# Kernel optimization log

Measured on AMD Instinct MI355X. Metric: run time of the kernel, lower is better.

Reference implementation:

```python
import jax, jax.numpy as jnp
import numpy as np

B, S, D, H = 2, 2048, 1024, 16
DK = D // H  # 64


def setup_inputs() -> dict:
    key = jax.random.key(0)
    ks = jax.random.split(key, 11)
    scale = 1.0 / np.sqrt(D)
    inp = {
        "x": jax.random.normal(ks[0], (B, S, D), dtype=jnp.float32),
        "z": jax.random.normal(ks[1], (B, S, D), dtype=jnp.float32),
        # causal mask, broadcast over batch and heads; masked_fill where mask==0
        "mask": jnp.tril(jnp.ones((1, 1, S, S), dtype=jnp.int32)),
        "wq_w": jax.random.normal(ks[2], (D, D), dtype=jnp.float32) * scale,
        "wq_b": jax.random.normal(ks[3], (D,), dtype=jnp.float32) * 0.01,
        "wk_w": jax.random.normal(ks[4], (D, D), dtype=jnp.float32) * scale,
        "wk_b": jax.random.normal(ks[5], (D,), dtype=jnp.float32) * 0.01,
        "wv_w": jax.random.normal(ks[6], (D, D), dtype=jnp.float32) * scale,
        "wv_b": jax.random.normal(ks[7], (D,), dtype=jnp.float32) * 0.01,
        "wo_w": jax.random.normal(ks[8], (D, D), dtype=jnp.float32) * scale,
        "wo_b": jax.random.normal(ks[9], (D,), dtype=jnp.float32) * 0.01,
    }
    return inp


def reference(x, z, mask, wq_w, wq_b, wk_w, wk_b, wv_w, wv_b, wo_w, wo_b):
    # torch Linear: y = x @ W.T + b
    q = x @ wq_w.T + wq_b
    k = z @ wk_w.T + wk_b
    # NOTE: faithful to source bug: value uses wk, not wv (wv is a dead param)
    v = z @ wk_w.T + wk_b

    def split_heads(t):  # [B,S,D] -> [B,H,S,DK]
        return t.reshape(B, S, H, DK).transpose(0, 2, 1, 3)

    q, k, v = split_heads(q), split_heads(k), split_heads(v)

    scores = jnp.einsum("bhqd,bhkd->bhqk", q, k) * (DK ** -0.5)
    scores = jnp.where(mask == 0, -jnp.inf, scores)
    attn_weights = jax.nn.softmax(scores, axis=-1)  # [B,H,S,S]
    atn = jnp.einsum("bhqk,bhkd->bhqd", attn_weights, v)

    concat = atn.transpose(0, 2, 1, 3).reshape(B, S, D)
    output = concat @ wo_w.T + wo_b  # dropout rate 0.0 -> identity
    concat_attn_weight = attn_weights.sum(axis=1)  # [B,S,S]
    return output, concat_attn_weight
```

## Files before the change

### kernel.cpp

```cpp
#include <hip/hip_runtime.h>

typedef __bf16 bf16_t;
typedef __bf16 bf16x4 __attribute__((ext_vector_type(4)));
typedef __bf16 bf16x8 __attribute__((ext_vector_type(8)));
typedef float  f32x4  __attribute__((ext_vector_type(4)));

#define MFMA(a, b, c) __builtin_amdgcn_mfma_f32_16x16x32_bf16((a), (b), (c), 0, 0, 0)

static constexpr int Bsz = 2, S = 2048, D = 1024, H = 16, DK = 64;
static constexpr float QSCALE = 0.125f * 1.4426950408889634f;

__device__ __forceinline__ float fexp2(float x) {
    return __builtin_amdgcn_exp2f(x);
}

__global__ __launch_bounds__(256) void cvt5(
    const float* __restrict__ x, const float* __restrict__ z,
    const float* __restrict__ wq, const float* __restrict__ wk,
    const float* __restrict__ wo,
    bf16_t* __restrict__ xb, bf16_t* __restrict__ zb,
    bf16_t* __restrict__ wqb, bf16_t* __restrict__ wkb, bf16_t* __restrict__ wob)
{
    constexpr int NXZ = Bsz * S * D / 4;
    constexpr int NW  = D * D / 4;
    int i = blockIdx.x * 256 + threadIdx.x;
    const float* s; bf16_t* d; int off;
    if (i < NXZ)                 { s = x;  d = xb;  off = i; }
    else if (i < 2 * NXZ)        { s = z;  d = zb;  off = i - NXZ; }
    else if (i < 2 * NXZ + NW)   { s = wq; d = wqb; off = i - 2 * NXZ; }
    else if (i < 2 * NXZ + 2*NW) { s = wk; d = wkb; off = i - 2 * NXZ - NW; }
    else                         { s = wo; d = wob; off = i - 2 * NXZ - 2 * NW; }
    float4 v = *(const float4*)&s[(size_t)off * 4];
    bf16x4 o;
    o[0] = (bf16_t)v.x; o[1] = (bf16_t)v.y; o[2] = (bf16_t)v.z; o[3] = (bf16_t)v.w;
    *(bf16x4*)&d[(size_t)off * 4] = o;
}

__global__ __launch_bounds__(512) void gemm_qk(
    const bf16_t* __restrict__ xA, const bf16_t* __restrict__ wqB,
    const float* __restrict__ wqb, bf16_t* __restrict__ Qc,
    const bf16_t* __restrict__ zA, const bf16_t* __restrict__ wkB,
    const float* __restrict__ wkb, bf16_t* __restrict__ Kc,
    bf16_t* __restrict__ KTout)
{
    constexpr int N = D, K = D;
    const int zi = blockIdx.z;
    const bf16_t* A    = zi ? zA  : xA;
    const bf16_t* B    = zi ? wkB : wqB;
    const float*  bias = zi ? wkb : wqb;
    bf16_t*       C    = zi ? Kc  : Qc;
    const float   sc   = zi ? 1.f : QSCALE;

    __shared__ bf16_t As[2][128][40];
    __shared__ bf16_t Bs[2][128][40];

    const int t    = threadIdx.x;
    const int wave = t >> 6, lane = t & 63;
    const int quad = lane >> 4, l15 = lane & 15;
    const int wm = (wave >> 1) * 32, wn = (wave & 1) * 64;
    const int rowbase = blockIdx.y * 128, colbase = blockIdx.x * 128;
    const int r  = t >> 2;
    const int cc = (t & 3) << 3;

    f32x4 acc[2][4];
#pragma unroll
    for (int i = 0; i < 2; ++i)
#pragma unroll
        for (int j = 0; j < 4; ++j) acc[i][j] = {0.f, 0.f, 0.f, 0.f};

    bf16x8 areg = *(const bf16x8*)&A[(size_t)(rowbase + r) * K + cc];
    bf16x8 breg = *(const bf16x8*)&B[(size_t)(colbase + r) * K + cc];
    *(bf16x8*)&As[0][r][cc] = areg;
    *(bf16x8*)&Bs[0][r][cc] = breg;
    __syncthreads();

    for (int kt = 0; kt < K; kt += 32) {
        const int cur = (kt >> 5) & 1, nxt = cur ^ 1;
        const bool more = (kt + 32) < K;
        if (more) {
            areg = *(const bf16x8*)&A[(size_t)(rowbase + r) * K + kt + 32 + cc];
            breg = *(const bf16x8*)&B[(size_t)(colbase + r) * K + kt + 32 + cc];
        }

        bf16x8 af[2], bfr[4];
#pragma unroll
        for (int mt = 0; mt < 2; ++mt)
            af[mt] = *(const bf16x8*)&As[cur][wm + mt * 16 + l15][quad * 8];
#pragma unroll
        for (int nt = 0; nt < 4; ++nt)
            bfr[nt] = *(const bf16x8*)&Bs[cur][wn + nt * 16 + l15][quad * 8];
#pragma unroll
        for (int mt = 0; mt < 2; ++mt)
#pragma unroll
            for (int nt = 0; nt < 4; ++nt)
                acc[mt][nt] = MFMA(af[mt], bfr[nt], acc[mt][nt]);

        if (more) {
            *(bf16x8*)&As[nxt][r][cc] = areg;
            *(bf16x8*)&Bs[nxt][r][cc] = breg;
        }
        __syncthreads();
    }

#pragma unroll
    for (int nt = 0; nt < 4; ++nt) {
        int col  = colbase + wn + nt * 16 + l15;
        float bv = bias[col];
#pragma unroll
        for (int mt = 0; mt < 2; ++mt) {
            int row0 = rowbase + wm + mt * 16 + quad * 4;
#pragma unroll
            for (int rr = 0; rr < 4; ++rr) {
                float v = (acc[mt][nt][rr] + bv) * sc;
                C[(size_t)(row0 + rr) * N + col] = (bf16_t)v;
                if (zi) {
                    int row = row0 + rr;
                    int bb = row >> 11, srow = row & (S - 1);
                    int hh = col >> 6,  dd   = col & 63;
                    KTout[(((size_t)bb * H + hh) * DK + dd) * S + srow] = (bf16_t)v;
                }
            }
        }
    }
}

__global__ __launch_bounds__(256) void gemm_obt(
    const bf16_t* __restrict__ A, const bf16_t* __restrict__ B,
    const float* __restrict__ bias, float* __restrict__ C)
{
    constexpr int N = D, K = D;
    __shared__ bf16_t As[2][64][40];
    __shared__ bf16_t Bs[2][128][40];

    const int t    = threadIdx.x;
    const int wave = t >> 6, lane = t & 63;
    const int quad = lane >> 4, l15 = lane & 15;
    const int wm = (wave >> 1) * 32, wn = (wave & 1) * 64;
    const int rowbase = blockIdx.y * 64, colbase = blockIdx.x * 128;
    const int r  = t >> 2;
    const int cc = (t & 3) << 3;

    f32x4 acc[2][4];
#pragma unroll
    for (int i = 0; i < 2; ++i)
#pragma unroll
        for (int j = 0; j < 4; ++j) acc[i][j] = {0.f, 0.f, 0.f, 0.f};

    bf16x8 areg  = *(const bf16x8*)&A[(size_t)(rowbase + r) * K + cc];
    bf16x8 breg0 = *(const bf16x8*)&B[(size_t)(colbase + r) * K + cc];
    bf16x8 breg1 = *(const bf16x8*)&B[(size_t)(colbase + 64 + r) * K + cc];
    *(bf16x8*)&As[0][r][cc]      = areg;
    *(bf16x8*)&Bs[0][r][cc]      = breg0;
    *(bf16x8*)&Bs[0][64 + r][cc] = breg1;
    __syncthreads();

    for (int kt = 0; kt < K; kt += 32) {
        const int cur = (kt >> 5) & 1, nxt = cur ^ 1;
        const bool more = (kt + 32) < K;
        if (more) {
            areg  = *(const bf16x8*)&A[(size_t)(rowbase + r) * K + kt + 32 + cc];
            breg0 = *(const bf16x8*)&B[(size_t)(colbase + r) * K + kt + 32 + cc];
            breg1 = *(const bf16x8*)&B[(size_t)(colbase + 64 + r) * K + kt + 32 + cc];
        }

        bf16x8 af[2], bfr[4];
#pragma unroll
        for (int mt = 0; mt < 2; ++mt)
            af[mt] = *(const bf16x8*)&As[cur][wm + mt * 16 + l15][quad * 8];
#pragma unroll
        for (int nt = 0; nt < 4; ++nt)
            bfr[nt] = *(const bf16x8*)&Bs[cur][wn + nt * 16 + l15][quad * 8];
#pragma unroll
        for (int mt = 0; mt < 2; ++mt)
#pragma unroll
            for (int nt = 0; nt < 4; ++nt)
                acc[mt][nt] = MFMA(af[mt], bfr[nt], acc[mt][nt]);

        if (more) {
            *(bf16x8*)&As[nxt][r][cc]      = areg;
            *(bf16x8*)&Bs[nxt][r][cc]      = breg0;
            *(bf16x8*)&Bs[nxt][64 + r][cc] = breg1;
        }
        __syncthreads();
    }

#pragma unroll
    for (int nt = 0; nt < 4; ++nt) {
        int col  = colbase + wn + nt * 16 + l15;
        float bv = bias[col];
#pragma unroll
        for (int mt = 0; mt < 2; ++mt) {
            int row0 = rowbase + wm + mt * 16 + quad * 4;
#pragma unroll
            for (int rr = 0; rr < 4; ++rr)
                C[(size_t)(row0 + rr) * N + col] = acc[mt][nt][rr] + bv;
        }
    }
}

__global__ __launch_bounds__(256) void attn_flash(
    const bf16_t* __restrict__ Q, const bf16_t* __restrict__ Km,
    const bf16_t* __restrict__ KT,
    bf16_t* __restrict__ Oc, float* __restrict__ il_ws)
{
    const int h = blockIdx.y, b = blockIdx.z;
    const int t = threadIdx.x;
    const int wave = t >> 6, lane = t & 63;
    const int quad = lane >> 4, l15 = lane & 15;

    __shared__ bf16_t Ks[2][64][72];
    __shared__ bf16_t KTs[2][64][72];
    __shared__ bf16_t PQ[64][72];

    const int hcol = h * DK;
    const bf16_t* KTh = KT + ((size_t)(b * H + h)) * DK * S;
    const size_t bS = (size_t)b * S;

    const int jr = (t >> 3);
    const int ce = (t & 7) * 8;
    const int iloc = wave * 16 + l15;

    for (int half = 0; half < 2; ++half) {
        const int qt = half == 0 ? (int)blockIdx.x : 31 - (int)blockIdx.x;
        const size_t qrow0 = bS + (size_t)qt * 64;

        __syncthreads();
        bf16x8 qld[2], kreg[2], ktreg[2];
#pragma unroll
        for (int p = 0; p < 2; ++p) {
            qld[p]   = *(const bf16x8*)&Q[(qrow0 + p * 32 + jr) * D + hcol + ce];
            kreg[p]  = *(const bf16x8*)&Km[(bS + p * 32 + jr) * D + hcol + ce];
            ktreg[p] = *(const bf16x8*)&KTh[(size_t)(p * 32 + jr) * S + ce];
        }
#pragma unroll
        for (int p = 0; p < 2; ++p) {
            *(bf16x8*)&PQ[p * 32 + jr][ce]     = qld[p];
            *(bf16x8*)&Ks[0][p * 32 + jr][ce]  = kreg[p];
            *(bf16x8*)&KTs[0][p * 32 + jr][ce] = ktreg[p];
        }
        __syncthreads();
        const bf16x8 qf0 = *(const bf16x8*)&PQ[wave * 16 + l15][quad * 8];
        const bf16x8 qf1 = *(const bf16x8*)&PQ[wave * 16 + l15][32 + quad * 8];

        f32x4 accO[4];
#pragma unroll
        for (int u = 0; u < 4; ++u) accO[u] = {0.f, 0.f, 0.f, 0.f};
        float l_part = 0.f;

        auto exp_pv = [&](f32x4 sv[4], int cur) {
#pragma unroll
            for (int nt = 0; nt < 4; ++nt)
#pragma unroll
                for (int r = 0; r < 4; ++r) {
                    float p = fexp2(sv[nt][r]);
                    sv[nt][r] = p;
                    l_part += p;
                }

#pragma unroll
            for (int nt = 0; nt < 4; ++nt) {
                bf16x4 pk;
                pk[0] = (bf16_t)sv[nt][0]; pk[1] = (bf16_t)sv[nt][1];
                pk[2] = (bf16_t)sv[nt][2]; pk[3] = (bf16_t)sv[nt][3];
                *(bf16x4*)&PQ[wave * 16 + l15][nt * 16 + quad * 4] = pk;
            }
            asm volatile("s_waitcnt lgkmcnt(0)" ::: "memory");

            bf16x8 pa0 = *(const bf16x8*)&PQ[wave * 16 + l15][quad * 8];
            bf16x8 pa1 = *(const bf16x8*)&PQ[wave * 16 + l15][32 + quad * 8];
#pragma unroll
            for (int u = 0; u < 4; ++u) {
                bf16x8 v0 = *(const bf16x8*)&KTs[cur][u * 16 + l15][quad * 8];
                bf16x8 v1 = *(const bf16x8*)&KTs[cur][u * 16 + l15][32 + quad * 8];
                accO[u] = MFMA(pa0, v0, accO[u]);
                accO[u] = MFMA(pa1, v1, accO[u]);
            }
        };

        for (int jt = 0; jt < qt; ++jt) {
            const int cur = jt & 1, nxt = cur ^ 1;
#pragma unroll
            for (int p = 0; p < 2; ++p) {
                kreg[p]  = *(const bf16x8*)&Km[(bS + (size_t)(jt + 1) * 64 + p * 32 + jr) * D + hcol + ce];
                ktreg[p] = *(const bf16x8*)&KTh[(size_t)(p * 32 + jr) * S + (size_t)(jt + 1) * 64 + ce];
            }

            f32x4 sv[4];
#pragma unroll
            for (int nt = 0; nt < 4; ++nt) {
                bf16x8 a0 = *(const bf16x8*)&Ks[cur][nt * 16 + l15][quad * 8];
                bf16x8 a1 = *(const bf16x8*)&Ks[cur][nt * 16 + l15][32 + quad * 8];
                f32x4 a = {0.f, 0.f, 0.f, 0.f};
                a = MFMA(a0, qf0, a);
                a = MFMA(a1, qf1, a);
                sv[nt] = a;
            }
            exp_pv(sv, cur);

#pragma unroll
            for (int p = 0; p < 2; ++p) {
                *(bf16x8*)&Ks[nxt][p * 32 + jr][ce]  = kreg[p];
                *(bf16x8*)&KTs[nxt][p * 32 + jr][ce] = ktreg[p];
            }
            __syncthreads();
        }

        {
            const int cur = qt & 1;
            f32x4 sv[4];
#pragma unroll
            for (int nt = 0; nt < 4; ++nt) {
                bf16x8 a0 = *(const bf16x8*)&Ks[cur][nt * 16 + l15][quad * 8];
                bf16x8 a1 = *(const bf16x8*)&Ks[cur][nt * 16 + l15][32 + quad * 8];
                f32x4 a = {0.f, 0.f, 0.f, 0.f};
                a = MFMA(a0, qf0, a);
                a = MFMA(a1, qf1, a);
#pragma unroll
                for (int r = 0; r < 4; ++r)
                    if ((nt * 16 + quad * 4 + r) > iloc) a[r] = -1e30f;
                sv[nt] = a;
            }
            exp_pv(sv, cur);
        }

        l_part += __shfl_xor(l_part, 16);
        l_part += __shfl_xor(l_part, 32);
        float invl = 1.f / l_part;
        float invl4[4];
#pragma unroll
        for (int r = 0; r < 4; ++r)
            invl4[r] = __shfl(invl, (quad << 4) + quad * 4 + r, 64);
#pragma unroll
        for (int u = 0; u < 4; ++u)
#pragma unroll
            for (int r = 0; r < 4; ++r)
                Oc[(qrow0 + wave * 16 + quad * 4 + r) * D + hcol + u * 16 + l15] =
                    (bf16_t)(accO[u][r] * invl4[r]);

        if (quad == 0) {
            size_t sb = ((size_t)(b * H + h)) * S + (size_t)qt * 64 + wave * 16 + l15;
            il_ws[sb] = invl;
        }
    }
}

__global__ __launch_bounds__(256) void attn_wsum(
    const bf16_t* __restrict__ Q, const bf16_t* __restrict__ Km,
    const float* __restrict__ il_ws, float* __restrict__ out2)
{
    const int jt = blockIdx.x, qt = blockIdx.y, b = blockIdx.z;
    const int t  = threadIdx.x;
    float* tile = out2 + (size_t)b * S * S + (size_t)qt * 64 * S + (size_t)jt * 64;

    if (jt > qt) {
        int r0 = t >> 2, c0 = (t & 3) * 16;
#pragma unroll
        for (int e = 0; e < 16; ++e) tile[(size_t)r0 * S + c0 + e] = 0.f;
        return;
    }

    const int wave = t >> 6, lane = t & 63;
    const int quad = lane >> 4, l15 = lane & 15;
    __shared__ bf16_t Ks[2][64][72];
    __shared__ bf16_t Qs[2][64][72];

    const int jr = (t >> 3), ce = (t & 7) * 8;
    const size_t krow = (size_t)b * S + (size_t)jt * 64;
    const size_t qrow = (size_t)b * S + (size_t)qt * 64;
    const bool diag = (jt == qt);

    f32x4 accs[4];
#pragma unroll
    for (int nt = 0; nt < 4; ++nt) accs[nt] = {0.f, 0.f, 0.f, 0.f};

    bf16x8 kreg[2], qreg[2];
#pragma unroll
    for (int p = 0; p < 2; ++p) {
        kreg[p] = *(const bf16x8*)&Km[(krow + p * 32 + jr) * D + ce];
        qreg[p] = *(const bf16x8*)&Q[(qrow + p * 32 + jr) * D + ce];
    }
#pragma unroll
    for (int p = 0; p < 2; ++p) {
        *(bf16x8*)&Ks[0][p * 32 + jr][ce] = kreg[p];
        *(bf16x8*)&Qs[0][p * 32 + jr][ce] = qreg[p];
    }
    __syncthreads();

    for (int h = 0; h < H; ++h) {
        const int cur = h & 1, nxt = cur ^ 1;

        if (h < H - 1) {
            const int hc = (h + 1) * DK;
#pragma unroll
            for (int p = 0; p < 2; ++p) {
                kreg[p] = *(const bf16x8*)&Km[(krow + p * 32 + jr) * D + hc + ce];
                qreg[p] = *(const bf16x8*)&Q[(qrow + p * 32 + jr) * D + hc + ce];
            }
        }

        bf16x8 qf0 = *(const bf16x8*)&Qs[cur][wave * 16 + l15][quad * 8];
        bf16x8 qf1 = *(const bf16x8*)&Qs[cur][wave * 16 + l15][32 + quad * 8];

        size_t mlb = ((size_t)(b * H + h)) * S + (size_t)qt * 64 + wave * 16 + quad * 4;
        f32x4 il = *(const f32x4*)&il_ws[mlb];

#pragma unroll
        for (int nt = 0; nt < 4; ++nt) {
            bf16x8 k0 = *(const bf16x8*)&Ks[cur][nt * 16 + l15][quad * 8];
            bf16x8 k1 = *(const bf16x8*)&Ks[cur][nt * 16 + l15][32 + quad * 8];
            f32x4 a = {0.f, 0.f, 0.f, 0.f};
            a = MFMA(qf0, k0, a);
            a = MFMA(qf1, k1, a);
            if (diag) {
#pragma unroll
                for (int r = 0; r < 4; ++r) {
                    int i = wave * 16 + quad * 4 + r;
                    int j = nt * 16 + l15;
                    float p = (j <= i) ? fexp2(a[r]) * il[r] : 0.f;
                    accs[nt][r] += p;
                }
            } else {
#pragma unroll
                for (int r = 0; r < 4; ++r)
                    accs[nt][r] += fexp2(a[r]) * il[r];
            }
        }

        if (h < H - 1) {
#pragma unroll
            for (int p = 0; p < 2; ++p) {
                *(bf16x8*)&Ks[nxt][p * 32 + jr][ce] = kreg[p];
                *(bf16x8*)&Qs[nxt][p * 32 + jr][ce] = qreg[p];
            }
        }
        __syncthreads();
    }

#pragma unroll
    for (int nt = 0; nt < 4; ++nt)
#pragma unroll
        for (int r = 0; r < 4; ++r)
            tile[(size_t)(wave * 16 + quad * 4 + r) * S + nt * 16 + l15] = accs[nt][r];
}

extern "C" void kernel_launch(void* const* d_in, const int* in_sizes, int n_in,
                              void* d_out, int out_size, void* d_ws, size_t ws_size,
                              hipStream_t stream)
{
    const float* x    = (const float*)d_in[0];
    const float* z    = (const float*)d_in[1];
    const float* wq_w = (const float*)d_in[3];
    const float* wq_b = (const float*)d_in[4];
    const float* wk_w = (const float*)d_in[5];
    const float* wk_b = (const float*)d_in[6];
    const float* wo_w = (const float*)d_in[9];
    const float* wo_b = (const float*)d_in[10];

    float* out  = (float*)d_out;
    float* out2 = out + (size_t)Bsz * S * D;

    float*  il_ws = (float*)d_ws;
    bf16_t* Qws   = (bf16_t*)(il_ws + (size_t)Bsz * H * S);
    bf16_t* Kws   = Qws + (size_t)Bsz * S * D;
    bf16_t* wq_bf = Kws + (size_t)Bsz * S * D;
    bf16_t* wk_bf = wq_bf + (size_t)D * D;
    bf16_t* wo_bf = wk_bf + (size_t)D * D;
    bf16_t* xb    = (bf16_t*)out;
    bf16_t* zb    = xb + (size_t)Bsz * S * D;
    bf16_t* Cc    = (bf16_t*)out2;
    bf16_t* KTws  = Cc + (size_t)Bsz * S * D;

    constexpr int CVT_BLOCKS = (2 * (Bsz * S * D / 4) + 3 * (D * D / 4)) / 256;
    cvt5<<<dim3(CVT_BLOCKS), dim3(256), 0, stream>>>(
        x, z, wq_w, wk_w, wo_w, xb, zb, wq_bf, wk_bf, wo_bf);
    gemm_qk<<<dim3(D / 128, (Bsz * S) / 128, 2), dim3(512), 0, stream>>>(
        xb, wq_bf, wq_b, Qws, zb, wk_bf, wk_b, Kws, KTws);
    attn_flash<<<dim3(S / 128, H, Bsz), dim3(256), 0, stream>>>(
        Qws, Kws, KTws, Cc, il_ws);
    gemm_obt<<<dim3(D / 128, (Bsz * S) / 64, 1), dim3(256), 0, stream>>>(
        Cc, wo_bf, wo_b, out);
    attn_wsum<<<dim3(S / 64, S / 64, Bsz), dim3(256), 0, stream>>>(
        Qws, Kws, il_ws, out2);
}
```

Measured before the change: 266.0 us.

## Fuse output projection and attention-weight sum into one launch

Merges the output-projection GEMM and the head-summed attention-weight kernel into a single launch whose block index selects which body to run. When the workspace is large enough, the concat buffer and K-transpose move into the workspace so they no longer alias out2, which makes running both tails concurrently safe. Separately, the weight-sum kernel now reads Q fragments straight from global memory into registers instead of staging them through shared memory. The aim is to cut one launch and its tail idle time and let the two tails overlap. In exchange the fused kernel reserves the larger shared-memory footprint for every block, which may lower occupancy for the weight-sum blocks.

```diff
diff --git a/kernel.cpp b/kernel.cpp
--- a/kernel.cpp
+++ b/kernel.cpp
@@ -124,19 +124,20 @@
     }
 }
 
-__global__ __launch_bounds__(256) void gemm_obt(
+__device__ __forceinline__ void obt_body(
+    int id, char* smem,
     const bf16_t* __restrict__ A, const bf16_t* __restrict__ B,
     const float* __restrict__ bias, float* __restrict__ C)
 {
     constexpr int N = D, K = D;
-    __shared__ bf16_t As[2][64][40];
-    __shared__ bf16_t Bs[2][128][40];
+    auto As = (bf16_t(*)[64][40])smem;
+    auto Bs = (bf16_t(*)[128][40])(smem + 10240);
 
     const int t    = threadIdx.x;
     const int wave = t >> 6, lane = t & 63;
     const int quad = lane >> 4, l15 = lane & 15;
     const int wm = (wave >> 1) * 32, wn = (wave & 1) * 64;
-    const int rowbase = blockIdx.y * 64, colbase = blockIdx.x * 128;
+    const int rowbase = (id >> 3) * 64, colbase = (id & 7) * 128;
     const int r  = t >> 2;
     const int cc = (t & 3) << 3;
 
@@ -198,6 +199,126 @@
     }
 }
 
+__device__ __forceinline__ void wsum_body(
+    int id, char* smem,
+    const bf16_t* __restrict__ Q, const bf16_t* __restrict__ Km,
+    const float* __restrict__ il_ws, float* __restrict__ out2)
+{
+    const int jt = id & 31, qt = (id >> 5) & 31, b = id >> 10;
+    const int t  = threadIdx.x;
+    float* tile = out2 + (size_t)b * S * S + (size_t)qt * 64 * S + (size_t)jt * 64;
+
+    if (jt > qt) {
+        int r0 = t >> 2, c0 = (t & 3) * 16;
+#pragma unroll
+        for (int e = 0; e < 16; ++e) tile[(size_t)r0 * S + c0 + e] = 0.f;
+        return;
+    }
+
+    const int wave = t >> 6, lane = t & 63;
+    const int quad = lane >> 4, l15 = lane & 15;
+    auto Ks = (bf16_t(*)[64][72])smem;
+
+    const int jr = (t >> 3), ce = (t & 7) * 8;
+    const size_t krow  = (size_t)b * S + (size_t)jt * 64;
+    const size_t qbase = ((size_t)b * S + (size_t)qt * 64 + wave * 16 + l15) * D + quad * 8;
+    const bool diag = (jt == qt);
+
+    f32x4 accs[4];
+#pragma unroll
+    for (int nt = 0; nt < 4; ++nt) accs[nt] = {0.f, 0.f, 0.f, 0.f};
+
+    bf16x8 kreg[2];
+#pragma unroll
+    for (int p = 0; p < 2; ++p)
+        kreg[p] = *(const bf16x8*)&Km[(krow + p * 32 + jr) * D + ce];
+    bf16x8 qf0 = *(const bf16x8*)&Q[qbase];
+    bf16x8 qf1 = *(const bf16x8*)&Q[qbase + 32];
+#pragma unroll
+    for (int p = 0; p < 2; ++p)
+        *(bf16x8*)&Ks[0][p * 32 + jr][ce] = kreg[p];
+    __syncthreads();
+
+    for (int h = 0; h < H; ++h) {
+        const int cur = h & 1, nxt = cur ^ 1;
+        bf16x8 qn0, qn1;
+        if (h < H - 1) {
+            const int hc = (h + 1) * DK;
+#pragma unroll
+            for (int p = 0; p < 2; ++p)
+                kreg[p] = *(const bf16x8*)&Km[(krow + p * 32 + jr) * D + hc + ce];
+            qn0 = *(const bf16x8*)&Q[qbase + hc];
+            qn1 = *(const bf16x8*)&Q[qbase + hc + 32];
+        }
+
+        size_t mlb = ((size_t)(b * H + h)) * S + (size_t)qt * 64 + wave * 16 + quad * 4;
+        f32x4 il = *(const f32x4*)&il_ws[mlb];
+
+#pragma unroll
+        for (int nt = 0; nt < 4; ++nt) {
+            bf16x8 k0 = *(const bf16x8*)&Ks[cur][nt * 16 + l15][quad * 8];
+            bf16x8 k1 = *(const bf16x8*)&Ks[cur][nt * 16 + l15][32 + quad * 8];
+            f32x4 a = {0.f, 0.f, 0.f, 0.f};
+            a = MFMA(qf0, k0, a);
+            a = MFMA(qf1, k1, a);
+            if (diag) {
+#pragma unroll
+                for (int r = 0; r < 4; ++r) {
+                    int i = wave * 16 + quad * 4 + r;
+                    int j = nt * 16 + l15;
+                    float p = (j <= i) ? fexp2(a[r]) * il[r] : 0.f;
+                    accs[nt][r] += p;
+                }
+            } else {
+#pragma unroll
+                for (int r = 0; r < 4; ++r)
+                    accs[nt][r] += fexp2(a[r]) * il[r];
+            }
+        }
+
+        if (h < H - 1) {
+#pragma unroll
+            for (int p = 0; p < 2; ++p)
+                *(bf16x8*)&Ks[nxt][p * 32 + jr][ce] = kreg[p];
+            qf0 = qn0; qf1 = qn1;
+        }
+        __syncthreads();
+    }
+
+#pragma unroll
+    for (int nt = 0; nt < 4; ++nt)
+#pragma unroll
+        for (int r = 0; r < 4; ++r)
+            tile[(size_t)(wave * 16 + quad * 4 + r) * S + nt * 16 + l15] = accs[nt][r];
+}
+
+__global__ __launch_bounds__(256) void tail_fused(
+    const bf16_t* __restrict__ Cc, const bf16_t* __restrict__ wo,
+    const float* __restrict__ wob, float* __restrict__ out,
+    const bf16_t* __restrict__ Q, const bf16_t* __restrict__ Km,
+    const float* __restrict__ il_ws, float* __restrict__ out2)
+{
+    __shared__ __align__(16) char smem[30720];
+    const int id = blockIdx.x;
+    if (id < 2048) wsum_body(id, smem, Q, Km, il_ws, out2);
+    else           obt_body(id - 2048, smem, Cc, wo, wob, out);
+}
+
+__global__ __launch_bounds__(256) void gemm_obt(
+    const bf16_t* __restrict__ A, const bf16_t* __restrict__ B,
+    const float* __restrict__ bias, float* __restrict__ C)
+{
+    __shared__ __align__(16) char smem[30720];
+    obt_body(blockIdx.x, smem, A, B, bias, C);
+}
+__global__ __launch_bounds__(256) void attn_wsum(
+    const bf16_t* __restrict__ Q, const bf16_t* __restrict__ Km,
+    const float* __restrict__ il_ws, float* __restrict__ out2)
+{
+    __shared__ __align__(16) char smem[18432];
+    wsum_body(blockIdx.x, smem, Q, Km, il_ws, out2);
+}
+
 __global__ __launch_bounds__(256) void attn_flash(
     const bf16_t* __restrict__ Q, const bf16_t* __restrict__ Km,
     const bf16_t* __restrict__ KT,
@@ -342,105 +463,6 @@
             il_ws[sb] = invl;
         }
     }
-}
-
-__global__ __launch_bounds__(256) void attn_wsum(
-    const bf16_t* __restrict__ Q, const bf16_t* __restrict__ Km,
-    const float* __restrict__ il_ws, float* __restrict__ out2)
-{
-    const int jt = blockIdx.x, qt = blockIdx.y, b = blockIdx.z;
-    const int t  = threadIdx.x;
-    float* tile = out2 + (size_t)b * S * S + (size_t)qt * 64 * S + (size_t)jt * 64;
-
-    if (jt > qt) {
-        int r0 = t >> 2, c0 = (t & 3) * 16;
-#pragma unroll
-        for (int e = 0; e < 16; ++e) tile[(size_t)r0 * S + c0 + e] = 0.f;
-        return;
-    }
-
-    const int wave = t >> 6, lane = t & 63;
-    const int quad = lane >> 4, l15 = lane & 15;
-    __shared__ bf16_t Ks[2][64][72];
-    __shared__ bf16_t Qs[2][64][72];
-
-    const int jr = (t >> 3), ce = (t & 7) * 8;
-    const size_t krow = (size_t)b * S + (size_t)jt * 64;
-    const size_t qrow = (size_t)b * S + (size_t)qt * 64;
-    const bool diag = (jt == qt);
-
-    f32x4 accs[4];
-#pragma unroll
-    for (int nt = 0; nt < 4; ++nt) accs[nt] = {0.f, 0.f, 0.f, 0.f};
-
-    bf16x8 kreg[2], qreg[2];
-#pragma unroll
-    for (int p = 0; p < 2; ++p) {
-        kreg[p] = *(const bf16x8*)&Km[(krow + p * 32 + jr) * D + ce];
-        qreg[p] = *(const bf16x8*)&Q[(qrow + p * 32 + jr) * D + ce];
-    }
-#pragma unroll
-    for (int p = 0; p < 2; ++p) {
-        *(bf16x8*)&Ks[0][p * 32 + jr][ce] = kreg[p];
-        *(bf16x8*)&Qs[0][p * 32 + jr][ce] = qreg[p];
-    }
-    __syncthreads();
-
-    for (int h = 0; h < H; ++h) {
-        const int cur = h & 1, nxt = cur ^ 1;
-
-        if (h < H - 1) {
-            const int hc = (h + 1) * DK;
-#pragma unroll
-            for (int p = 0; p < 2; ++p) {
-                kreg[p] = *(const bf16x8*)&Km[(krow + p * 32 + jr) * D + hc + ce];
-                qreg[p] = *(const bf16x8*)&Q[(qrow + p * 32 + jr) * D + hc + ce];
-            }
-        }
-
-        bf16x8 qf0 = *(const bf16x8*)&Qs[cur][wave * 16 + l15][quad * 8];
-        bf16x8 qf1 = *(const bf16x8*)&Qs[cur][wave * 16 + l15][32 + quad * 8];
-
-        size_t mlb = ((size_t)(b * H + h)) * S + (size_t)qt * 64 + wave * 16 + quad * 4;
-        f32x4 il = *(const f32x4*)&il_ws[mlb];
-
-#pragma unroll
-        for (int nt = 0; nt < 4; ++nt) {
-            bf16x8 k0 = *(const bf16x8*)&Ks[cur][nt * 16 + l15][quad * 8];
-            bf16x8 k1 = *(const bf16x8*)&Ks[cur][nt * 16 + l15][32 + quad * 8];
-            f32x4 a = {0.f, 0.f, 0.f, 0.f};
-            a = MFMA(qf0, k0, a);
-            a = MFMA(qf1, k1, a);
-            if (diag) {
-#pragma unroll
-                for (int r = 0; r < 4; ++r) {
-                    int i = wave * 16 + quad * 4 + r;
-                    int j = nt * 16 + l15;
-                    float p = (j <= i) ? fexp2(a[r]) * il[r] : 0.f;
-                    accs[nt][r] += p;
-                }
-            } else {
-#pragma unroll
-                for (int r = 0; r < 4; ++r)
-                    accs[nt][r] += fexp2(a[r]) * il[r];
-            }
-        }
-
-        if (h < H - 1) {
-#pragma unroll
-            for (int p = 0; p < 2; ++p) {
-                *(bf16x8*)&Ks[nxt][p * 32 + jr][ce] = kreg[p];
-                *(bf16x8*)&Qs[nxt][p * 32 + jr][ce] = qreg[p];
-            }
-        }
-        __syncthreads();
-    }
-
-#pragma unroll
-    for (int nt = 0; nt < 4; ++nt)
-#pragma unroll
-        for (int r = 0; r < 4; ++r)
-            tile[(size_t)(wave * 16 + quad * 4 + r) * S + nt * 16 + l15] = accs[nt][r];
 }
 
 extern "C" void kernel_launch(void* const* d_in, const int* in_sizes, int n_in,
@@ -465,10 +487,15 @@
     bf16_t* wq_bf = Kws + (size_t)Bsz * S * D;
     bf16_t* wk_bf = wq_bf + (size_t)D * D;
     bf16_t* wo_bf = wk_bf + (size_t)D * D;
+    bf16_t* ws_end = wo_bf + (size_t)D * D;
     bf16_t* xb    = (bf16_t*)out;
     bf16_t* zb    = xb + (size_t)Bsz * S * D;
-    bf16_t* Cc    = (bf16_t*)out2;
-    bf16_t* KTws  = Cc + (size_t)Bsz * S * D;
+
+    const size_t needed = ((size_t)((char*)ws_end - (char*)d_ws))
+                        + 2 * (size_t)Bsz * S * D * sizeof(bf16_t);
+    const bool fused = ws_size >= needed;
+    bf16_t* Cc   = fused ? ws_end : (bf16_t*)out2;
+    bf16_t* KTws = Cc + (size_t)Bsz * S * D;
 
     constexpr int CVT_BLOCKS = (2 * (Bsz * S * D / 4) + 3 * (D * D / 4)) / 256;
     cvt5<<<dim3(CVT_BLOCKS), dim3(256), 0, stream>>>(
@@ -477,8 +504,11 @@
         xb, wq_bf, wq_b, Qws, zb, wk_bf, wk_b, Kws, KTws);
     attn_flash<<<dim3(S / 128, H, Bsz), dim3(256), 0, stream>>>(
         Qws, Kws, KTws, Cc, il_ws);
-    gemm_obt<<<dim3(D / 128, (Bsz * S) / 64, 1), dim3(256), 0, stream>>>(
-        Cc, wo_bf, wo_b, out);
-    attn_wsum<<<dim3(S / 64, S / 64, Bsz), dim3(256), 0, stream>>>(
-        Qws, Kws, il_ws, out2);
-}
+    if (fused) {
+        tail_fused<<<dim3(2048 + 512), dim3(256), 0, stream>>>(
+            Cc, wo_bf, wo_b, out, Qws, Kws, il_ws, out2);
+    } else {
+        gemm_obt<<<dim3(512), dim3(256), 0, stream>>>(Cc, wo_bf, wo_b, out);
+        attn_wsum<<<dim3(2048), dim3(256), 0, stream>>>(Qws, Kws, il_ws, out2);
+    }
+}
```

Measured after the change: 267.4 us. Within noise of the previous version (+0.5%).
